# Optimization experiments

Hardware: AMD Instinct MI355X
Metric: run time of the kernel (lower is better)

The kernel has to match this reference:

```python
import jax, jax.numpy as jnp
import numpy as np

DIM = 384
NH = 12
HEAD = DIM // NH
WS = (7, 7, 7)
L = WS[0] * WS[1] * WS[2]          # 343 tokens per window
NW = 64                             # number of windows (mask.shape[0])
B = 1                               # batch per window group
N = B * NW                          # leading dim of x
TBL = (2 * WS[0] - 1) * (2 * WS[1] - 1) * (2 * WS[2] - 1)  # 2197
SCALE = HEAD ** -0.5


def _rel_index():
    # Standard Swin 3D relative position index, shape (L, L), values in [0, TBL)
    coords = np.stack(np.meshgrid(*[np.arange(w) for w in WS], indexing='ij')).reshape(3, -1)  # (3, L)
    rel = coords[:, :, None] - coords[:, None, :]                     # (3, L, L)
    rel = rel + (np.array(WS) - 1)[:, None, None]                     # shift to >= 0
    s1 = (2 * WS[1] - 1) * (2 * WS[2] - 1)
    s2 = (2 * WS[2] - 1)
    idx = rel[0] * s1 + rel[1] * s2 + rel[2]
    return jnp.asarray(idx, jnp.int32)


def setup_inputs() -> dict:
    key = jax.random.key(0)
    k_x, k_m, k_qkv, k_tbl, k_pw = jax.random.split(key, 5)
    x = jax.random.normal(k_x, (N, L, DIM), dtype=jnp.float32)
    mask = jax.random.bernoulli(k_m, 0.5, (NW, L, L))                 # bool, True = masked
    qkv_w = jax.random.normal(k_qkv, (DIM, 3 * DIM), dtype=jnp.float32) * 0.02
    table = jax.random.normal(k_tbl, (TBL, NH), dtype=jnp.float32) * 0.02
    proj_w = jax.random.normal(k_pw, (DIM, DIM), dtype=jnp.float32) * 0.02
    proj_b = jnp.zeros((DIM,), dtype=jnp.float32)
    rel_idx = _rel_index()
    return {"x": x, "qkv_w": qkv_w, "table": table, "proj_w": proj_w,
            "proj_b": proj_b, "mask": mask, "rel_idx": rel_idx}


def reference(x, qkv_w, table, proj_w, proj_b, mask, rel_idx):
    n, l, _ = x.shape
    # QKV projection (no bias, qkv_bias=False)
    qkv = (x @ qkv_w).reshape(n, l, 3, NH, HEAD).transpose(2, 0, 3, 1, 4)  # (3, n, nh, l, ch)
    q, k, v = qkv[0], qkv[1], qkv[2]
    attn = jnp.einsum('nhlc,nhmc->nhlm', q * SCALE, k)                 # (n, nh, l, l)
    # gather relative position bias: (L*L, nh) -> (nh, L, L)
    bias = table[rel_idx.reshape(-1)].reshape(l, l, NH).transpose(2, 0, 1)
    attn = attn + bias[None]
    # per-window boolean mask: attn viewed as (batch, nw, nh, l, l)
    attn = attn.reshape(-1, NW, NH, l, l)
    attn = jnp.where(mask[None, :, None], -jnp.inf, attn).reshape(n, NH, l, l)
    attn = jax.nn.softmax(attn, axis=-1)
    out = jnp.einsum('nhlm,nhmc->nhlc', attn, v)                       # (n, nh, l, ch)
    out = out.transpose(0, 2, 1, 3).reshape(n, l, DIM)
    return out @ proj_w + proj_b
```

## Files before the change

### kernel.cpp

```cpp
#include <hip/hip_runtime.h>


#define DIMD 384
#define NHH 12
#define HEADD 32
#define LL 343
#define NWW 64
#define NTOK (NWW * LL)
#define MPT 176
#define MP (MPT * 128)
#define LP 352
#define QT 22
#define MW 12
#define CSS 136
#define SCALE_ 0.17677669529663687f
#define LOG2E_ 1.4426950408889634f
#define NEGBIG_ (-1.0e4f)

typedef _Float16 f16;
typedef _Float16 v8h __attribute__((ext_vector_type(8)));
typedef _Float16 v4h __attribute__((ext_vector_type(4)));
typedef float v4f __attribute__((ext_vector_type(4)));

__device__ __forceinline__ void async_cp16(const void* g, void* l) {
    __builtin_amdgcn_global_load_lds(
        (const __attribute__((address_space(1))) void*)g,
        (__attribute__((address_space(3))) void*)l, 16, 0, 0);
}

__device__ __forceinline__ unsigned int pk2(float a, float b) {
    return __builtin_bit_cast(unsigned int, __builtin_amdgcn_cvt_pkrtz(a, b));
}

constexpr size_t HBUF = (size_t)NHH * MP * HEADD * 2;
constexpr size_t OFF_Q    = 0;
constexpr size_t OFF_K    = OFF_Q  + HBUF;
constexpr size_t OFF_V    = OFF_K  + HBUF;
constexpr size_t OFF_AO   = OFF_V  + HBUF;
constexpr size_t OFF_BT   = OFF_AO + (size_t)MP * DIMD * 2;
constexpr size_t OFF_WT   = OFF_BT + (size_t)NHH * LP * LP * 4;
constexpr size_t OFF_PWT  = OFF_WT + (size_t)3 * DIMD * DIMD * 2;
constexpr size_t OFF_MTB  = OFF_PWT + (size_t)DIMD * DIMD * 2;

constexpr int SMEM_ATTN = (LP * 32 + 32 * LP + 8 * 16 * 32) * 2;

#define S0 (NTOK * DIMD / 4)
#define S1 (3 * DIMD * DIMD)
#define S2 (DIMD * DIMD)
#define S3 (NHH * LP * LP)
#define S4 (NWW * MW * LP)
#define SPREP (S0 + S1 + S2 + S3 + S4)

__global__ __launch_bounds__(256) void prep_all(
    const float* __restrict__ x, f16* __restrict__ xh,
    const float* __restrict__ qkv_w, f16* __restrict__ wt,
    const float* __restrict__ proj_w, f16* __restrict__ pwt,
    const float* __restrict__ table, const int* __restrict__ rel, float* __restrict__ btf,
    const int* __restrict__ mask, unsigned int* __restrict__ mtb) {
    int t = blockIdx.x * 256 + threadIdx.x;
    if (t < S0) {
        float4 v = *(const float4*)(x + (size_t)t * 4);
        v4h o; o[0] = (f16)v.x; o[1] = (f16)v.y; o[2] = (f16)v.z; o[3] = (f16)v.w;
        *(v4h*)(xh + (size_t)t * 4) = o;
    } else if (t < S0 + S1) {
        int e = t - S0;
        int n = e / DIMD, k = e % DIMD;
        wt[e] = (f16)qkv_w[(size_t)k * (3 * DIMD) + n];
    } else if (t < S0 + S1 + S2) {
        int e = t - S0 - S1;
        int n = e / DIMD, k = e % DIMD;
        pwt[e] = (f16)proj_w[(size_t)k * DIMD + n];
    } else if (t < S0 + S1 + S2 + S3) {
        int e = t - S0 - S1 - S2;
        int h = e / (LP * LP), rem = e % (LP * LP);
        int kq = rem / (LP * 4);
        int rem2 = rem % (LP * 4);
        int col = rem2 >> 2, e2 = rem2 & 3;
        int key = kq * 4 + e2;
        float v = NEGBIG_;
        if (col < LL && key < LL) v = table[(size_t)rel[col * LL + key] * NHH + h] * LOG2E_;
        btf[e] = v;
    } else if (t < SPREP) {
        int e = t - S0 - S1 - S2 - S3;
        int n = e / (MW * LP), rem = e % (MW * LP);
        int q = rem / MW, kw = rem % MW;
        unsigned int wd = 0;
        if (q < LL && kw < 11) {
            int kbase = kw * 32;
            int kmax = LL - kbase; if (kmax > 32) kmax = 32;
            const int* mrow = mask + ((size_t)n * LL + q) * LL + kbase;
#pragma unroll 4
            for (int b = 0; b < kmax; ++b)
                if (mrow[b]) wd |= (1u << b);
        }
        mtb[((size_t)n * LP + q) * MW + kw] = wd;
    }
}

__global__ __launch_bounds__(256) void qkv_gemm(
    const f16* __restrict__ xh, const f16* __restrict__ wt,
    f16* __restrict__ qb, f16* __restrict__ kb, f16* __restrict__ vb) {
    __shared__ f16 ABs[8192];
    f16* As = ABs;
    f16* Bs = ABs + 4096;
    const int lin = blockIdx.x;
    const int m0 = ((lin / 72) * 8 + (lin & 7)) * 128;
    const int n0 = ((lin >> 3) % 9) * 128;
    const int tid = threadIdx.x;
    const int wave = tid >> 6, lane = tid & 63;
    const int quad = lane >> 4, l15 = lane & 15;
    const int wm = (wave >> 1) * 64, wn = (wave & 1) * 64;
    const int srow = (lane >> 2);
    const int scol = (lane & 3) * 8;
    const f16* ga0 = xh + (size_t)(m0 + wave * 32 + srow) * DIMD + scol;
    const f16* ga1 = xh + (size_t)(m0 + wave * 32 + 16 + srow) * DIMD + scol;
    const f16* gb0 = wt + (size_t)(n0 + wave * 32 + srow) * DIMD + scol;
    const f16* gb1 = wt + (size_t)(n0 + wave * 32 + 16 + srow) * DIMD + scol;
    f16* la0 = As + (wave * 2) * 512;
    f16* la1 = As + (wave * 2 + 1) * 512;
    f16* lb0 = Bs + (wave * 2) * 512;
    f16* lb1 = Bs + (wave * 2 + 1) * 512;
    v4f acc[4][4] = {};
    for (int k0 = 0; k0 < DIMD; k0 += 32) {
        async_cp16(ga0 + k0, la0);
        async_cp16(ga1 + k0, la1);
        async_cp16(gb0 + k0, lb0);
        async_cp16(gb1 + k0, lb1);
        __syncthreads();
        v8h a[4], b[4];
#pragma unroll
        for (int i = 0; i < 4; ++i) a[i] = *(const v8h*)(As + (wm + i * 16 + l15) * 32 + quad * 8);
#pragma unroll
        for (int j = 0; j < 4; ++j) b[j] = *(const v8h*)(Bs + (wn + j * 16 + l15) * 32 + quad * 8);
#pragma unroll
        for (int i = 0; i < 4; ++i)
#pragma unroll
            for (int j = 0; j < 4; ++j)
                acc[i][j] = __builtin_amdgcn_mfma_f32_16x16x32_f16(a[i], b[j], acc[i][j], 0, 0, 0);
        __syncthreads();
    }
    const int t = n0 / DIMD;
    f16* dst = (t == 0) ? qb : (t == 1) ? kb : vb;
    const float sc = (t == 0) ? (SCALE_ * LOG2E_) : 1.0f;
    const int nrel = n0 - t * DIMD;
    f16* Cs = ABs;
    const int rl0 = (wave >> 1) * 16 + quad * 4;
#pragma unroll
    for (int i = 0; i < 4; ++i) {
#pragma unroll
        for (int e = 0; e < 4; ++e)
#pragma unroll
            for (int j = 0; j < 4; ++j)
                Cs[(rl0 + e) * CSS + wn + j * 16 + l15] = (f16)(acc[i][j][e] * sc);
        __syncthreads();
#pragma unroll
        for (int c = 0; c < 2; ++c) {
            int idx = c * 256 + tid;
            int rl = idx >> 4, col8 = (idx & 15) * 8;
            int gm = m0 + ((rl < 16) ? (i * 16 + rl) : (48 + i * 16 + rl));
            if (gm < NTOK) {
                int col = nrel + col8;
                size_t off = (size_t)(col >> 5) * ((size_t)MP * HEADD)
                           + (col & 31) + (size_t)gm * HEADD;
                *(v8h*)(dst + off) = *(const v8h*)(Cs + rl * CSS + col8);
            }
        }
        __syncthreads();
    }
}

__global__ __launch_bounds__(512, 6) void attn_kernel(
    const f16* __restrict__ qb, const f16* __restrict__ kb, const f16* __restrict__ vb,
    const float* __restrict__ biasT, const unsigned int* __restrict__ mtb,
    f16* __restrict__ ao) {
    extern __shared__ char smem[];
    f16* Ks  = (f16*)smem;
    f16* Vts = Ks + LP * 32;
    f16* Ps  = Vts + 32 * LP;
    const int bid = blockIdx.x;
    const int j2 = (bid & 7) * 96 + (bid >> 3);
    const int n = j2 & 63, h = j2 >> 6;
    const int tid = threadIdx.x, wave = tid >> 6, lane = tid & 63;
    const int quad = lane >> 4, l15 = lane & 15;
    const size_t slice = ((size_t)h * MP + n * LL) * HEADD;
    const f16* qg = qb + slice;
    const f16* kg = kb + slice;
    const f16* vg = vb + slice;
    for (int i = tid; i < LP * 4; i += 512) {
        int row = i >> 2, c8 = i & 3;
        v8h vv = {};
        if (row < LL) vv = *(const v8h*)(kg + (size_t)i * 8);
        *(v8h*)(Ks + row * 32 + ((c8 ^ (row & 3)) << 3)) = vv;
    }
    for (int i = tid; i < LP * 8; i += 512) {
        int key = i >> 3, c4 = (i & 7) * 4;
        ushort4 vv = make_ushort4(0, 0, 0, 0);
        if (key < LL) vv = *(const ushort4*)(vg + (size_t)key * HEADD + c4);
        int blk = key >> 3, off = key & 7;
        Vts[(c4 + 0) * LP + ((blk ^ 0) << 3) + off] = *(const f16*)&vv.x;
        Vts[(c4 + 1) * LP + ((blk ^ 1) << 3) + off] = *(const f16*)&vv.y;
        Vts[(c4 + 2) * LP + ((blk ^ 2) << 3) + off] = *(const f16*)&vv.z;
        Vts[(c4 + 3) * LP + ((blk ^ 3) << 3) + off] = *(const f16*)&vv.w;
    }
    __syncthreads();
    f16* Pw = Ps + wave * (16 * 32);
    const float* bh = biasT + (size_t)h * LP * LP;
    const unsigned int* mg = mtb + (size_t)n * LP * MW;
    const v8h ones = {(f16)1.f, (f16)1.f, (f16)1.f, (f16)1.f,
                      (f16)1.f, (f16)1.f, (f16)1.f, (f16)1.f};
    const int pswz = (l15 >> 1) & 3;
    const int kswz = (quad ^ (l15 & 3)) << 3;
    for (int qt = wave; qt < QT; qt += 8) {
        const int q = qt * 16 + l15;
        v8h af = *(const v8h*)(qg + (size_t)q * HEADD + quad * 8);
        uint4 mA = *(const uint4*)(mg + q * MW);
        uint4 mB = *(const uint4*)(mg + q * MW + 4);
        uint4 mC = *(const uint4*)(mg + q * MW + 8);
        unsigned int m[12] = {mA.x, mA.y, mA.z, mA.w, mB.x, mB.y, mB.z, mB.w,
                              mC.x, mC.y, mC.z, mC.w};
        const float* bq = bh + (size_t)q * 4;
        v4f cinN[2];
        cinN[0] = *(const v4f*)(bq + (size_t)(quad) * (LP * 4));
        cinN[1] = *(const v4f*)(bq + (size_t)(4 + quad) * (LP * 4));
        v4f o0 = {}, o1 = {}, o2 = {};
#pragma unroll
        for (int ktp = 0; ktp < 11; ++ktp) {
            v4f cin0 = cinN[0], cin1 = cinN[1];
            if (ktp < 10) {
                cinN[0] = *(const v4f*)(bq + (size_t)((ktp + 1) * 8 + quad) * (LP * 4));
                cinN[1] = *(const v4f*)(bq + (size_t)((ktp + 1) * 8 + 4 + quad) * (LP * 4));
            }
            v8h bf0 = *(const v8h*)(Ks + (ktp * 32 + l15) * 32 + kswz);
            v8h bf1 = *(const v8h*)(Ks + (ktp * 32 + 16 + l15) * 32 + kswz);
            unsigned int mw = m[ktp];
            unsigned int mb0 = mw >> (quad * 4);
            unsigned int mb1 = mw >> (quad * 4 + 16);
#pragma unroll
            for (int e = 0; e < 4; ++e) {
                if ((mb0 >> e) & 1u) cin0[e] = NEGBIG_;
                if ((mb1 >> e) & 1u) cin1[e] = NEGBIG_;
            }
            v4f s0 = __builtin_amdgcn_mfma_f32_16x16x32_f16(bf0, af, cin0, 0, 0, 0);
            v4f s1 = __builtin_amdgcn_mfma_f32_16x16x32_f16(bf1, af, cin1, 0, 0, 0);
            unsigned int u0 = pk2(__builtin_amdgcn_exp2f(s0[0]), __builtin_amdgcn_exp2f(s0[1]));
            unsigned int u1 = pk2(__builtin_amdgcn_exp2f(s0[2]), __builtin_amdgcn_exp2f(s0[3]));
            unsigned int u2 = pk2(__builtin_amdgcn_exp2f(s1[0]), __builtin_amdgcn_exp2f(s1[1]));
            unsigned int u3 = pk2(__builtin_amdgcn_exp2f(s1[2]), __builtin_amdgcn_exp2f(s1[3]));
            f16* pr = Pw + l15 * 32 + (quad & 1) * 4;
            *(uint2*)(pr + ((((quad >> 1) + 0) ^ pswz) << 3)) = make_uint2(u0, u1);
            *(uint2*)(pr + ((((quad >> 1) + 2) ^ pswz) << 3)) = make_uint2(u2, u3);
            v8h a = *(const v8h*)(Pw + l15 * 32 + ((quad ^ pswz) << 3));
            int vblk = ((ktp * 4 + quad) ^ (l15 & 3)) << 3;
            v8h w0 = *(const v8h*)(Vts + l15 * LP + vblk);
            v8h w1 = *(const v8h*)(Vts + (16 + l15) * LP + vblk);
            o0 = __builtin_amdgcn_mfma_f32_16x16x32_f16(w0, a, o0, 0, 0, 0);
            o1 = __builtin_amdgcn_mfma_f32_16x16x32_f16(w1, a, o1, 0, 0, 0);
            o2 = __builtin_amdgcn_mfma_f32_16x16x32_f16(ones, a, o2, 0, 0, 0);
        }
        if (q < LL) {
            float inv = 1.0f / o2[0];
            f16* orow = ao + ((size_t)(n * LL + q)) * DIMD + h * HEADD + quad * 4;
            v4h w0, w1;
#pragma unroll
            for (int e = 0; e < 4; ++e) {
                w0[e] = (f16)(o0[e] * inv);
                w1[e] = (f16)(o1[e] * inv);
            }
            *(v4h*)(orow) = w0;
            *(v4h*)(orow + 16) = w1;
        }
    }
}

__global__ __launch_bounds__(256) void proj_gemm(
    const f16* __restrict__ ao, const f16* __restrict__ pwt,
    const float* __restrict__ pb, float* __restrict__ out) {
    __shared__ f16 As[128 * 32];
    __shared__ f16 Bs[128 * 32];
    const int lin = blockIdx.x;
    const int m0 = ((lin / 24) * 8 + (lin & 7)) * 128;
    const int n0 = ((lin >> 3) % 3) * 128;
    const int tid = threadIdx.x;
    const int wave = tid >> 6, lane = tid & 63;
    const int quad = lane >> 4, l15 = lane & 15;
    const int wm = (wave >> 1) * 64, wn = (wave & 1) * 64;
    const int srow = (lane >> 2);
    const int scol = (lane & 3) * 8;
    const f16* ga0 = ao + (size_t)(m0 + wave * 32 + srow) * DIMD + scol;
    const f16* ga1 = ao + (size_t)(m0 + wave * 32 + 16 + srow) * DIMD + scol;
    const f16* gb0 = pwt + (size_t)(n0 + wave * 32 + srow) * DIMD + scol;
    const f16* gb1 = pwt + (size_t)(n0 + wave * 32 + 16 + srow) * DIMD + scol;
    f16* la0 = As + (wave * 2) * 512;
    f16* la1 = As + (wave * 2 + 1) * 512;
    f16* lb0 = Bs + (wave * 2) * 512;
    f16* lb1 = Bs + (wave * 2 + 1) * 512;
    v4f acc[4][4] = {};
    for (int k0 = 0; k0 < DIMD; k0 += 32) {
        async_cp16(ga0 + k0, la0);
        async_cp16(ga1 + k0, la1);
        async_cp16(gb0 + k0, lb0);
        async_cp16(gb1 + k0, lb1);
        __syncthreads();
        v8h a[4], b[4];
#pragma unroll
        for (int i = 0; i < 4; ++i) a[i] = *(const v8h*)(As + (wm + i * 16 + l15) * 32 + quad * 8);
#pragma unroll
        for (int j = 0; j < 4; ++j) b[j] = *(const v8h*)(Bs + (wn + j * 16 + l15) * 32 + quad * 8);
#pragma unroll
        for (int i = 0; i < 4; ++i)
#pragma unroll
            for (int j = 0; j < 4; ++j)
                acc[i][j] = __builtin_amdgcn_mfma_f32_16x16x32_f16(a[i], b[j], acc[i][j], 0, 0, 0);
        __syncthreads();
    }
#pragma unroll
    for (int i = 0; i < 4; ++i)
#pragma unroll
        for (int e = 0; e < 4; ++e) {
            int gm = m0 + wm + i * 16 + quad * 4 + e;
            if (gm < NTOK) {
#pragma unroll
                for (int j = 0; j < 4; ++j) {
                    int gn = n0 + wn + j * 16 + l15;
                    out[(size_t)gm * DIMD + gn] = acc[i][j][e] + pb[gn];
                }
            }
        }
}

extern "C" void kernel_launch(void* const* d_in, const int* in_sizes, int n_in,
                              void* d_out, int out_size, void* d_ws, size_t ws_size,
                              hipStream_t stream) {
    const float* x      = (const float*)d_in[0];
    const float* qkv_w  = (const float*)d_in[1];
    const float* table  = (const float*)d_in[2];
    const float* proj_w = (const float*)d_in[3];
    const float* proj_b = (const float*)d_in[4];
    const int* mask     = (const int*)d_in[5];
    const int* rel      = (const int*)d_in[6];
    float* out = (float*)d_out;
    char* ws = (char*)d_ws;

    f16* q    = (f16*)(ws + OFF_Q);
    f16* k    = (f16*)(ws + OFF_K);
    f16* v    = (f16*)(ws + OFF_V);
    f16* xh   = (f16*)(ws + OFF_AO);
    f16* ao   = (f16*)(ws + OFF_AO);
    float* bt = (float*)(ws + OFF_BT);
    f16* wt   = (f16*)(ws + OFF_WT);
    f16* pwt  = (f16*)(ws + OFF_PWT);
    unsigned int* mtb = (unsigned int*)(ws + OFF_MTB);

    (void)hipFuncSetAttribute((const void*)attn_kernel,
                              hipFuncAttributeMaxDynamicSharedMemorySize, SMEM_ATTN);

    prep_all<<<(SPREP + 255) / 256, 256, 0, stream>>>(
        x, xh, qkv_w, wt, proj_w, pwt, table, rel, bt, mask, mtb);
    qkv_gemm<<<dim3(MPT * 9), 256, 0, stream>>>(xh, wt, q, k, v);
    attn_kernel<<<dim3(NWW * NHH), 512, SMEM_ATTN, stream>>>(q, k, v, bt, mtb, ao);
    proj_gemm<<<dim3(MPT * 3), 256, 0, stream>>>(ao, pwt, proj_b, out);
}
```

Measured before the change: 219.1 us.

## Double-buffer GEMM K-loop, register-shuffle P in attention, per-wave epilogue staging

After: 397.5 us. 1.81x slower.

```diff
diff --git a/kernel.cpp b/kernel.cpp
--- a/kernel.cpp
+++ b/kernel.cpp
@@ -12,7 +12,6 @@
 #define LP 352
 #define QT 22
 #define MW 12
-#define CSS 136
 #define SCALE_ 0.17677669529663687f
 #define LOG2E_ 1.4426950408889634f
 #define NEGBIG_ (-1.0e4f)
@@ -21,6 +20,7 @@
 typedef _Float16 v8h __attribute__((ext_vector_type(8)));
 typedef _Float16 v4h __attribute__((ext_vector_type(4)));
 typedef float v4f __attribute__((ext_vector_type(4)));
+typedef unsigned int v2u __attribute__((ext_vector_type(2)));
 
 __device__ __forceinline__ void async_cp16(const void* g, void* l) {
     __builtin_amdgcn_global_load_lds(
@@ -42,7 +42,7 @@
 constexpr size_t OFF_PWT  = OFF_WT + (size_t)3 * DIMD * DIMD * 2;
 constexpr size_t OFF_MTB  = OFF_PWT + (size_t)DIMD * DIMD * 2;
 
-constexpr int SMEM_ATTN = (LP * 32 + 32 * LP + 8 * 16 * 32) * 2;
+constexpr int SMEM_ATTN = (LP * 32 + LP * 32) * 2;
 
 #define S0 (NTOK * DIMD / 4)
 #define S1 (3 * DIMD * DIMD)
@@ -100,9 +100,7 @@
 __global__ __launch_bounds__(256) void qkv_gemm(
     const f16* __restrict__ xh, const f16* __restrict__ wt,
     f16* __restrict__ qb, f16* __restrict__ kb, f16* __restrict__ vb) {
-    __shared__ f16 ABs[8192];
-    f16* As = ABs;
-    f16* Bs = ABs + 4096;
+    __shared__ f16 ABs[16384];
     const int lin = blockIdx.x;
     const int m0 = ((lin / 72) * 8 + (lin & 7)) * 128;
     const int n0 = ((lin >> 3) % 9) * 128;
@@ -110,23 +108,32 @@
     const int wave = tid >> 6, lane = tid & 63;
     const int quad = lane >> 4, l15 = lane & 15;
     const int wm = (wave >> 1) * 64, wn = (wave & 1) * 64;
-    const int srow = (lane >> 2);
-    const int scol = (lane & 3) * 8;
+    const int srow = lane >> 2, scol = (lane & 3) * 8;
     const f16* ga0 = xh + (size_t)(m0 + wave * 32 + srow) * DIMD + scol;
-    const f16* ga1 = xh + (size_t)(m0 + wave * 32 + 16 + srow) * DIMD + scol;
+    const f16* ga1 = ga0 + (size_t)16 * DIMD;
     const f16* gb0 = wt + (size_t)(n0 + wave * 32 + srow) * DIMD + scol;
-    const f16* gb1 = wt + (size_t)(n0 + wave * 32 + 16 + srow) * DIMD + scol;
-    f16* la0 = As + (wave * 2) * 512;
-    f16* la1 = As + (wave * 2 + 1) * 512;
-    f16* lb0 = Bs + (wave * 2) * 512;
-    f16* lb1 = Bs + (wave * 2 + 1) * 512;
+    const f16* gb1 = gb0 + (size_t)16 * DIMD;
+    {
+        f16* la = ABs + wave * 1024;
+        async_cp16(ga0, la);
+        async_cp16(ga1, la + 512);
+        async_cp16(gb0, la + 4096);
+        async_cp16(gb1, la + 4096 + 512);
+    }
+    __syncthreads();
     v4f acc[4][4] = {};
-    for (int k0 = 0; k0 < DIMD; k0 += 32) {
-        async_cp16(ga0 + k0, la0);
-        async_cp16(ga1 + k0, la1);
-        async_cp16(gb0 + k0, lb0);
-        async_cp16(gb1 + k0, lb1);
-        __syncthreads();
+    for (int t = 0; t < 12; ++t) {
+        const int cur = (t & 1) << 13;
+        if (t < 11) {
+            const int nk = (t + 1) * 32;
+            f16* la = ABs + (cur ^ 8192) + wave * 1024;
+            async_cp16(ga0 + nk, la);
+            async_cp16(ga1 + nk, la + 512);
+            async_cp16(gb0 + nk, la + 4096);
+            async_cp16(gb1 + nk, la + 4096 + 512);
+        }
+        const f16* As = ABs + cur;
+        const f16* Bs = As + 4096;
         v8h a[4], b[4];
 #pragma unroll
         for (int i = 0; i < 4; ++i) a[i] = *(const v8h*)(As + (wm + i * 16 + l15) * 32 + quad * 8);
@@ -139,33 +146,29 @@
                 acc[i][j] = __builtin_amdgcn_mfma_f32_16x16x32_f16(a[i], b[j], acc[i][j], 0, 0, 0);
         __syncthreads();
     }
-    const int t = n0 / DIMD;
-    f16* dst = (t == 0) ? qb : (t == 1) ? kb : vb;
-    const float sc = (t == 0) ? (SCALE_ * LOG2E_) : 1.0f;
-    const int nrel = n0 - t * DIMD;
-    f16* Cs = ABs;
-    const int rl0 = (wave >> 1) * 16 + quad * 4;
+    const int t3 = n0 / DIMD;
+    f16* dst = (t3 == 0) ? qb : (t3 == 1) ? kb : vb;
+    const float sc = (t3 == 0) ? (SCALE_ * LOG2E_) : 1.0f;
+    const int nrel = n0 - t3 * DIMD;
+    f16* Cw = ABs + wave * (16 * 72);
 #pragma unroll
     for (int i = 0; i < 4; ++i) {
 #pragma unroll
         for (int e = 0; e < 4; ++e)
 #pragma unroll
             for (int j = 0; j < 4; ++j)
-                Cs[(rl0 + e) * CSS + wn + j * 16 + l15] = (f16)(acc[i][j][e] * sc);
-        __syncthreads();
+                Cw[(quad * 4 + e) * 72 + j * 16 + l15] = (f16)(acc[i][j][e] * sc);
 #pragma unroll
         for (int c = 0; c < 2; ++c) {
-            int idx = c * 256 + tid;
-            int rl = idx >> 4, col8 = (idx & 15) * 8;
-            int gm = m0 + ((rl < 16) ? (i * 16 + rl) : (48 + i * 16 + rl));
+            int chunk = quad + c * 4;
+            int gm = m0 + wm + i * 16 + l15;
+            int gcol = nrel + wn + chunk * 8;
             if (gm < NTOK) {
-                int col = nrel + col8;
-                size_t off = (size_t)(col >> 5) * ((size_t)MP * HEADD)
-                           + (col & 31) + (size_t)gm * HEADD;
-                *(v8h*)(dst + off) = *(const v8h*)(Cs + rl * CSS + col8);
-            }
-        }
-        __syncthreads();
+                size_t off = (size_t)(gcol >> 5) * ((size_t)MP * HEADD)
+                           + (gcol & 31) + (size_t)gm * HEADD;
+                *(v8h*)(dst + off) = *(const v8h*)(Cw + l15 * 72 + chunk * 8);
+            }
+        }
     }
 }
 
@@ -176,7 +179,6 @@
     extern __shared__ char smem[];
     f16* Ks  = (f16*)smem;
     f16* Vts = Ks + LP * 32;
-    f16* Ps  = Vts + 32 * LP;
     const int bid = blockIdx.x;
     const int j2 = (bid & 7) * 96 + (bid >> 3);
     const int n = j2 & 63, h = j2 >> 6;
@@ -192,24 +194,22 @@
         if (row < LL) vv = *(const v8h*)(kg + (size_t)i * 8);
         *(v8h*)(Ks + row * 32 + ((c8 ^ (row & 3)) << 3)) = vv;
     }
-    for (int i = tid; i < LP * 8; i += 512) {
-        int key = i >> 3, c4 = (i & 7) * 4;
-        ushort4 vv = make_ushort4(0, 0, 0, 0);
-        if (key < LL) vv = *(const ushort4*)(vg + (size_t)key * HEADD + c4);
-        int blk = key >> 3, off = key & 7;
-        Vts[(c4 + 0) * LP + ((blk ^ 0) << 3) + off] = *(const f16*)&vv.x;
-        Vts[(c4 + 1) * LP + ((blk ^ 1) << 3) + off] = *(const f16*)&vv.y;
-        Vts[(c4 + 2) * LP + ((blk ^ 2) << 3) + off] = *(const f16*)&vv.z;
-        Vts[(c4 + 3) * LP + ((blk ^ 3) << 3) + off] = *(const f16*)&vv.w;
+    for (int i = tid; i < LP * 4; i += 512) {
+        int key = i >> 2, c8 = i & 3;
+        v8h vv = {};
+        if (key < LL) vv = *(const v8h*)(vg + (size_t)key * HEADD + c8 * 8);
+        int kk = key & 31;
+        f16* d = Vts + (key >> 5) * 1024 + ((((kk >> 3) ^ c8) & 3) << 3) + (kk & 7);
+#pragma unroll
+        for (int j = 0; j < 8; ++j) d[(c8 * 8 + j) * 32] = vv[j];
     }
     __syncthreads();
-    f16* Pw = Ps + wave * (16 * 32);
     const float* bh = biasT + (size_t)h * LP * LP;
     const unsigned int* mg = mtb + (size_t)n * LP * MW;
     const v8h ones = {(f16)1.f, (f16)1.f, (f16)1.f, (f16)1.f,
                       (f16)1.f, (f16)1.f, (f16)1.f, (f16)1.f};
-    const int pswz = (l15 >> 1) & 3;
     const int kswz = (quad ^ (l15 & 3)) << 3;
+    const int xw = (l15 >> 3) & 1;
     for (int qt = wave; qt < QT; qt += 8) {
         const int q = qt * 16 + l15;
         v8h af = *(const v8h*)(qg + (size_t)q * HEADD + quad * 8);
@@ -242,17 +242,19 @@
             }
             v4f s0 = __builtin_amdgcn_mfma_f32_16x16x32_f16(bf0, af, cin0, 0, 0, 0);
             v4f s1 = __builtin_amdgcn_mfma_f32_16x16x32_f16(bf1, af, cin1, 0, 0, 0);
-            unsigned int u0 = pk2(__builtin_amdgcn_exp2f(s0[0]), __builtin_amdgcn_exp2f(s0[1]));
-            unsigned int u1 = pk2(__builtin_amdgcn_exp2f(s0[2]), __builtin_amdgcn_exp2f(s0[3]));
-            unsigned int u2 = pk2(__builtin_amdgcn_exp2f(s1[0]), __builtin_amdgcn_exp2f(s1[1]));
-            unsigned int u3 = pk2(__builtin_amdgcn_exp2f(s1[2]), __builtin_amdgcn_exp2f(s1[3]));
-            f16* pr = Pw + l15 * 32 + (quad & 1) * 4;
-            *(uint2*)(pr + ((((quad >> 1) + 0) ^ pswz) << 3)) = make_uint2(u0, u1);
-            *(uint2*)(pr + ((((quad >> 1) + 2) ^ pswz) << 3)) = make_uint2(u2, u3);
-            v8h a = *(const v8h*)(Pw + l15 * 32 + ((quad ^ pswz) << 3));
-            int vblk = ((ktp * 4 + quad) ^ (l15 & 3)) << 3;
-            v8h w0 = *(const v8h*)(Vts + l15 * LP + vblk);
-            v8h w1 = *(const v8h*)(Vts + (16 + l15) * LP + vblk);
+            unsigned int x0 = pk2(__builtin_amdgcn_exp2f(s0[0]), __builtin_amdgcn_exp2f(s0[1]));
+            unsigned int x1 = pk2(__builtin_amdgcn_exp2f(s0[2]), __builtin_amdgcn_exp2f(s0[3]));
+            unsigned int y0 = pk2(__builtin_amdgcn_exp2f(s1[0]), __builtin_amdgcn_exp2f(s1[1]));
+            unsigned int y1 = pk2(__builtin_amdgcn_exp2f(s1[2]), __builtin_amdgcn_exp2f(s1[3]));
+            v2u r0 = __builtin_amdgcn_permlane32_swap(x0, y0, false, false);
+            v2u r1 = __builtin_amdgcn_permlane16_swap(r0[0], r0[1], false, false);
+            v2u r2 = __builtin_amdgcn_permlane32_swap(x1, y1, false, false);
+            v2u r3 = __builtin_amdgcn_permlane16_swap(r2[0], r2[1], false, false);
+            uint4 av = make_uint4(r1[0], r3[0], r1[1], r3[1]);
+            v8h a = __builtin_bit_cast(v8h, av);
+            const f16* vt = Vts + ktp * 1024;
+            v8h w0 = *(const v8h*)(vt + l15 * 32 + ((quad ^ xw) << 3));
+            v8h w1 = *(const v8h*)(vt + (16 + l15) * 32 + ((quad ^ 2 ^ xw) << 3));
             o0 = __builtin_amdgcn_mfma_f32_16x16x32_f16(w0, a, o0, 0, 0, 0);
             o1 = __builtin_amdgcn_mfma_f32_16x16x32_f16(w1, a, o1, 0, 0, 0);
             o2 = __builtin_amdgcn_mfma_f32_16x16x32_f16(ones, a, o2, 0, 0, 0);
@@ -275,8 +277,7 @@
 __global__ __launch_bounds__(256) void proj_gemm(
     const f16* __restrict__ ao, const f16* __restrict__ pwt,
     const float* __restrict__ pb, float* __restrict__ out) {
-    __shared__ f16 As[128 * 32];
-    __shared__ f16 Bs[128 * 32];
+    __shared__ f16 ABs[16384];
     const int lin = blockIdx.x;
     const int m0 = ((lin / 24) * 8 + (lin & 7)) * 128;
     const int n0 = ((lin >> 3) % 3) * 128;
@@ -284,23 +285,32 @@
     const int wave = tid >> 6, lane = tid & 63;
     const int quad = lane >> 4, l15 = lane & 15;
     const int wm = (wave >> 1) * 64, wn = (wave & 1) * 64;
-    const int srow = (lane >> 2);
-    const int scol = (lane & 3) * 8;
+    const int srow = lane >> 2, scol = (lane & 3) * 8;
     const f16* ga0 = ao + (size_t)(m0 + wave * 32 + srow) * DIMD + scol;
-    const f16* ga1 = ao + (size_t)(m0 + wave * 32 + 16 + srow) * DIMD + scol;
+    const f16* ga1 = ga0 + (size_t)16 * DIMD;
     const f16* gb0 = pwt + (size_t)(n0 + wave * 32 + srow) * DIMD + scol;
-    const f16* gb1 = pwt + (size_t)(n0 + wave * 32 + 16 + srow) * DIMD + scol;
-    f16* la0 = As + (wave * 2) * 512;
-    f16* la1 = As + (wave * 2 + 1) * 512;
-    f16* lb0 = Bs + (wave * 2) * 512;
-    f16* lb1 = Bs + (wave * 2 + 1) * 512;
+    const f16* gb1 = gb0 + (size_t)16 * DIMD;
+    {
+        f16* la = ABs + wave * 1024;
+        async_cp16(ga0, la);
+        async_cp16(ga1, la + 512);
+        async_cp16(gb0, la + 4096);
+        async_cp16(gb1, la + 4096 + 512);
+    }
+    __syncthreads();
     v4f acc[4][4] = {};
-    for (int k0 = 0; k0 < DIMD; k0 += 32) {
-        async_cp16(ga0 + k0, la0);
-        async_cp16(ga1 + k0, la1);
-        async_cp16(gb0 + k0, lb0);
-        async_cp16(gb1 + k0, lb1);
-        __syncthreads();
+    for (int t = 0; t < 12; ++t) {
+        const int cur = (t & 1) << 13;
+        if (t < 11) {
+            const int nk = (t + 1) * 32;
+            f16* la = ABs + (cur ^ 8192) + wave * 1024;
+            async_cp16(ga0 + nk, la);
+            async_cp16(ga1 + nk, la + 512);
+            async_cp16(gb0 + nk, la + 4096);
+            async_cp16(gb1 + nk, la + 4096 + 512);
+        }
+        const f16* As = ABs + cur;
+        const f16* Bs = As + 4096;
         v8h a[4], b[4];
 #pragma unroll
         for (int i = 0; i < 4; ++i) a[i] = *(const v8h*)(As + (wm + i * 16 + l15) * 32 + quad * 8);
```
